# Kernel optimization log

Hardware: AMD Instinct MI355X
Metric: run time of the kernel (lower is better)

The kernel has to match this reference:

```python
import jax, jax.numpy as jnp
import numpy as np

DEPTH = 4
SCALE = 1.0


def _exp_levels(v, depth):
    # Tensor-algebra exponential of a linear segment with increment v: level k = v^{(x)k} / k!
    # v: (B, C); returns tuple of (B, C^k) for k=1..depth
    B = v.shape[0]
    levels = [v]
    for k in range(2, depth + 1):
        levels.append((levels[-1][:, :, None] * v[:, None, :]).reshape(B, -1) / k)
    return tuple(levels)


def _chen_step(levels, v, depth):
    # Chen's identity: S_new = S (x) exp(v), flattened per level.
    e = _exp_levels(v, depth)
    B = v.shape[0]
    new = []
    for k in range(1, depth + 1):
        acc = levels[k - 1] + e[k - 1]
        for i in range(1, k):
            acc = acc + (levels[i - 1][:, :, None] * e[k - i - 1][:, None, :]).reshape(B, -1)
        new.append(acc)
    return tuple(new)


def signature(path, depth):
    # path: (B, T, C) -> concatenated signature levels (B, C + C^2 + ... + C^depth)
    dx = path[:, 1:] - path[:, :-1]          # (B, T-1, C)
    init = _exp_levels(dx[:, 0], depth)      # signature of first segment
    rest = jnp.moveaxis(dx[:, 1:], 0, 1)     # (T-2, B, C)

    def step(lv, v):
        return _chen_step(lv, v, depth), None

    final, _ = jax.lax.scan(step, init, rest)
    return jnp.concatenate(final, axis=-1)


def setup_inputs() -> dict:
    key = jax.random.key(0)
    k1, k2, k3 = jax.random.split(key, 3)
    N, B, T, C = 4096, 1024, 256, 10
    original = jax.random.normal(k1, (N, T, C), dtype=jnp.float32) * 0.1
    generated = jax.random.normal(k2, (B, T, C), dtype=jnp.float32) * 0.1
    sample_idx = jax.random.permutation(k3, N)[:B].astype(jnp.int64)  # sample without replacement
    return {"original": original, "generated": generated, "sample_idx": sample_idx}


def reference(original, generated, sample_idx):
    sig_orig = signature(original, DEPTH)                  # (N, D)
    selected = sig_orig[sample_idx]                        # (B, D)
    sig_gen = signature(generated, DEPTH)                  # (B, D)
    diff = jnp.mean(selected, axis=0) - jnp.mean(sig_gen, axis=0)
    return jnp.linalg.norm(diff) * SCALE
```

## Files before the change

kernel.cpp:

```cpp
#include <hip/hip_runtime.h>

#define T_LEN 256
#define C_DIM 10
#define NSTEP 255
#define BSZ   1024
#define NPAIR 1024
#define D1 10
#define D2 100
#define D3 1000
#define DTOT 11110
#define PATH_ELEMS (T_LEN * C_DIM)
#define DX_ELEMS (NSTEP * C_DIM)
#define DXROW 12

typedef float f32x2 __attribute__((ext_vector_type(2)));
typedef float f32x4 __attribute__((ext_vector_type(4)));

#define PK_FMA(d, a, b) \
    asm("v_pk_fma_f32 %0, %1, %2, %0" : "+v"(d) : "v"(a), "v"(b))
#define PK_FMA_B0(d, a, b) \
    asm("v_pk_fma_f32 %0, %1, %2, %0 op_sel:[0,0,0] op_sel_hi:[0,1,1]" \
        : "+v"(d) : "v"(a), "v"(b))
#define PK_FMA_B1(d, a, b) \
    asm("v_pk_fma_f32 %0, %1, %2, %0 op_sel:[1,0,0] op_sel_hi:[1,1,1]" \
        : "+v"(d) : "v"(a), "v"(b))
#define PK_FMA_B0N(d, a, b, c) \
    asm("v_pk_fma_f32 %0, %1, %2, %3 op_sel:[0,0,0] op_sel_hi:[0,1,1]" \
        : "=v"(d) : "v"(a), "v"(b), "v"(c))
#define PK_FMA_B1N(d, a, b, c) \
    asm("v_pk_fma_f32 %0, %1, %2, %3 op_sel:[1,0,0] op_sel_hi:[1,1,1]" \
        : "=v"(d) : "v"(a), "v"(b), "v"(c))
#define PK_FMA_S1B0N(d, a, b, c) \
    asm("v_pk_fma_f32 %0, %1, %2, %3 op_sel:[0,0,0] op_sel_hi:[1,0,1]" \
        : "=v"(d) : "v"(a), "v"(b), "v"(c))
#define PK_FMA_S1B1N(d, a, b, c) \
    asm("v_pk_fma_f32 %0, %1, %2, %3 op_sel:[0,1,0] op_sel_hi:[1,1,1]" \
        : "=v"(d) : "v"(a), "v"(b), "v"(c))
#define PK_FMA_S1B0(d, a, b) \
    asm("v_pk_fma_f32 %0, %1, %2, %0 op_sel:[0,0,0] op_sel_hi:[1,0,1]" \
        : "+v"(d) : "v"(a), "v"(b))
#define PK_FMA_S1B1(d, a, b) \
    asm("v_pk_fma_f32 %0, %1, %2, %0 op_sel:[0,1,0] op_sel_hi:[1,1,1]" \
        : "+v"(d) : "v"(a), "v"(b))
#define PK_MUL_HALF(d, a) \
    asm("v_pk_mul_f32 %0, %1, 0.5 op_sel:[0,0] op_sel_hi:[1,0]" \
        : "=v"(d) : "v"(a))

__global__ __launch_bounds__(256)
void sig_accum_kernel(
    const float* __restrict__ original,
    const float* __restrict__ generated,
    const int* __restrict__ sample_idx,
    float* __restrict__ ws, int nrep, int store_mode)
{
    const int tid  = threadIdx.x;
    const int bp   = blockIdx.x;
    const int b    = bp >> 1;
    const int pass = bp & 1;
    const float sgn = pass ? 1.0f : -1.0f;

    __shared__ float s_dx[NSTEP * DXROW];

    const float* path = pass
        ? original + (size_t)sample_idx[b] * PATH_ELEMS
        : generated + (size_t)b * PATH_ELEMS;

    for (int idx = tid; idx < DX_ELEMS; idx += 256) {
        int t = idx / C_DIM, c = idx - t * C_DIM;
        s_dx[t * DXROW + c] = path[idx + C_DIM] - path[idx];
    }
    __syncthreads();

    const int mbase = 2 * tid;
    const int k0  = mbase / 100;
    const int ij0 = mbase - k0 * 100;
    const int ia  = ij0 / 10;
    const int j0  = ij0 - ia * 10;

    float s1a = 0.0f;
    f32x2 s2p = {0.0f, 0.0f};
    f32x2 s3p[2] = {{0.0f, 0.0f}, {0.0f, 0.0f}};
    f32x2 acc2[4][5];
    #pragma unroll
    for (int r = 0; r < 4; ++r)
        #pragma unroll
        for (int i = 0; i < 5; ++i) acc2[r][i] = (f32x2){0.0f, 0.0f};

    if (tid < 250) {
        const float* vrow = s_dx;
        #pragma unroll 2
        for (int t = 0; t < NSTEP; ++t, vrow += DXROW) {
            const f32x4 va = *(const f32x4*)(vrow);
            const f32x4 vb = *(const f32x4*)(vrow + 4);
            const f32x2 vc = *(const f32x2*)(vrow + 8);
            const f32x2 vjp = *(const f32x2*)(vrow + j0);
            const float via = vrow[ia];
            f32x2 vkp;
            vkp.x = vrow[k0];
            vkp.y = vrow[k0 + 5];

            const f32x2 vv2[5] = {va.xy, va.zw, vb.xy, vb.zw, vc};

            const float t3  = fmaf(via, 0.5f, s1a);
            const float t1b = fmaf(via, 0.25f, s1a) * (1.0f / 3.0f);
            const float t2b = fmaf(via, (1.0f / 3.0f), s1a) * 0.5f;
            f32x2 pA; pA.x = t1b; pA.y = t2b;
            f32x2 pT; pT.x = t3;  pT.y = t3;

            f32x2 vkhp;
            PK_MUL_HALF(vkhp, vkp);

            f32x2 a2p, b2p;
            PK_FMA_B0N(a2p, pA, vjp, s2p);
            PK_FMA_B1N(b2p, pA, vjp, s2p);
            PK_FMA_B0(s2p, pT, vjp);

            f32x2 a3xp, a3yp;
            PK_FMA_S1B0N(a3xp, a2p, vkhp, s3p[0]);
            PK_FMA_S1B1N(a3yp, a2p, vkhp, s3p[1]);
            PK_FMA_S1B0(s3p[0], b2p, vkp);
            PK_FMA_S1B1(s3p[1], b2p, vkp);

            #pragma unroll
            for (int i = 0; i < 5; ++i) {
                PK_FMA_B0(acc2[0][i], a3xp, vv2[i]);
                PK_FMA_B1(acc2[1][i], a3xp, vv2[i]);
                PK_FMA_B0(acc2[2][i], a3yp, vv2[i]);
                PK_FMA_B1(acc2[3][i], a3yp, vv2[i]);
            }
            s1a += via;
        }
    }

    if (store_mode) {
        float* row = ws + (size_t)bp * DTOT;
        if (tid < D1)
            row[tid] = sgn * (path[(T_LEN - 1) * C_DIM + tid] - path[tid]);
        if (tid < 50) {
            row[D1 + ij0]     = sgn * s2p[0];
            row[D1 + ij0 + 1] = sgn * s2p[1];
        }
        if (tid < 250) {
            #pragma unroll
            for (int ch = 0; ch < 2; ++ch) {
                const int kk = k0 + 5 * ch;
                #pragma unroll
                for (int q = 0; q < 2; ++q) {
                    const int idx3 = (ij0 + q) * 10 + kk;
                    row[D1 + D2 + idx3] = sgn * s3p[ch][q];
                    float* p4 = row + D1 + D2 + D3 + (size_t)idx3 * 10;
                    #pragma unroll
                    for (int i = 0; i < 5; ++i)
                        *(f32x2*)&p4[2 * i] = sgn * acc2[ch * 2 + q][i];
                }
            }
        }
    } else {
        float* base = ws + (size_t)(b % nrep) * DTOT;
        if (tid < D1)
            atomicAdd(&base[tid],
                      sgn * (path[(T_LEN - 1) * C_DIM + tid] - path[tid]));
        if (tid < 50) {
            atomicAdd(&base[D1 + ij0],     sgn * s2p[0]);
            atomicAdd(&base[D1 + ij0 + 1], sgn * s2p[1]);
        }
        if (tid < 250) {
            #pragma unroll
            for (int ch = 0; ch < 2; ++ch) {
                const int kk = k0 + 5 * ch;
                #pragma unroll
                for (int q = 0; q < 2; ++q) {
                    const int idx3 = (ij0 + q) * 10 + kk;
                    atomicAdd(&base[D1 + D2 + idx3], sgn * s3p[ch][q]);
                    #pragma unroll
                    for (int l = 0; l < 10; ++l)
                        atomicAdd(&base[D1 + D2 + D3 + idx3 * 10 + l],
                                  sgn * acc2[ch * 2 + q][l >> 1][l & 1]);
                }
            }
        }
    }
}

__global__ __launch_bounds__(256) void sig_sum_kernel(
    const float* __restrict__ ws, float* __restrict__ accvec)
{
    const int d2 = blockIdx.x * 256 + threadIdx.x;
    if (d2 >= DTOT / 2) return;
    const float* p = ws + (size_t)(blockIdx.y * 32) * DTOT + 2 * d2;
    float sx = 0.0f, sy = 0.0f;
    #pragma unroll
    for (int r = 0; r < 32; ++r) {
        const float2 v = *(const float2*)(p + (size_t)r * DTOT);
        sx += v.x; sy += v.y;
    }
    atomicAdd(&accvec[2 * d2], sx);
    atomicAdd(&accvec[2 * d2 + 1], sy);
}

__global__ __launch_bounds__(256) void sig_sumsq_kernel(
    const float* __restrict__ accvec, float* __restrict__ sumsq,
    unsigned int* __restrict__ counter, float* __restrict__ out, int nblocks)
{
    const int d = blockIdx.x * 256 + threadIdx.x;
    float s = 0.0f;
    if (d < DTOT) { float v = accvec[d]; s = v * v; }
    for (int off = 32; off > 0; off >>= 1) s += __shfl_down(s, off, 64);
    __shared__ float red[4];
    __shared__ unsigned int lastflag;
    if ((threadIdx.x & 63) == 0) red[threadIdx.x >> 6] = s;
    __syncthreads();
    if (threadIdx.x == 0) {
        atomicAdd(sumsq, red[0] + red[1] + red[2] + red[3]);
        __threadfence();
        lastflag = (atomicAdd(counter, 1u) == (unsigned int)(nblocks - 1));
    }
    __syncthreads();
    if (threadIdx.x == 0 && lastflag) {
        __threadfence();
        out[0] = sqrtf(*(volatile float*)sumsq) * (1.0f / (float)BSZ);
    }
}

__global__ __launch_bounds__(256) void sig_reduce_kernel(
    const float* __restrict__ ws, int nrows, float* __restrict__ sumsq,
    unsigned int* __restrict__ counter, float* __restrict__ out, int nblocks)
{
    const int d = blockIdx.x * 256 + threadIdx.x;
    float s = 0.0f;
    if (d < DTOT) {
        for (int r = 0; r < nrows; ++r) s += ws[(size_t)r * DTOT + d];
        s = s * s;
    }
    for (int off = 32; off > 0; off >>= 1) s += __shfl_down(s, off, 64);
    __shared__ float red[4];
    __shared__ unsigned int lastflag;
    if ((threadIdx.x & 63) == 0) red[threadIdx.x >> 6] = s;
    __syncthreads();
    if (threadIdx.x == 0) {
        atomicAdd(sumsq, red[0] + red[1] + red[2] + red[3]);
        __threadfence();
        lastflag = (atomicAdd(counter, 1u) == (unsigned int)(nblocks - 1));
    }
    __syncthreads();
    if (threadIdx.x == 0 && lastflag) {
        __threadfence();
        out[0] = sqrtf(*(volatile float*)sumsq) * (1.0f / (float)BSZ);
    }
}

extern "C" void kernel_launch(void* const* d_in, const int* in_sizes, int n_in,
                              void* d_out, int out_size, void* d_ws, size_t ws_size,
                              hipStream_t stream) {
    const float* original   = (const float*)d_in[0];
    const float* generated  = (const float*)d_in[1];
    const int*   sample_idx = (const int*)d_in[2];
    float* out = (float*)d_out;
    float* ws  = (float*)d_ws;

    const size_t need_split = ((size_t)(2 * NPAIR + 1) * DTOT + 2) * sizeof(float);
    const size_t need_store = ((size_t)(NPAIR + 1) * DTOT + 2) * sizeof(float);

    if (ws_size >= need_split) {
        float* accvec = ws + (size_t)2 * NPAIR * DTOT;
        float* sumsq  = accvec + DTOT;
        unsigned int* counter = (unsigned int*)(sumsq + 1);
        hipMemsetAsync(accvec, 0, (DTOT + 2) * sizeof(float), stream);
        sig_accum_kernel<<<2 * NPAIR, 256, 0, stream>>>(original, generated,
                                                        sample_idx, ws, 1, 1);
        dim3 g1((DTOT / 2 + 255) / 256, 2 * NPAIR / 32);
        sig_sum_kernel<<<g1, 256, 0, stream>>>(ws, accvec);
        const int nb2 = (DTOT + 255) / 256;
        sig_sumsq_kernel<<<nb2, 256, 0, stream>>>(accvec, sumsq, counter, out, nb2);
    } else if (ws_size >= need_store) {
        float* accvec = ws + (size_t)NPAIR * DTOT;
        float* sumsq  = accvec + DTOT;
        unsigned int* counter = (unsigned int*)(sumsq + 1);
        hipMemsetAsync(ws, 0, need_store, stream);
        sig_accum_kernel<<<2 * NPAIR, 256, 0, stream>>>(original, generated,
                                                        sample_idx, ws, NPAIR, 0);
        dim3 g1((DTOT / 2 + 255) / 256, NPAIR / 32);
        sig_sum_kernel<<<g1, 256, 0, stream>>>(ws, accvec);
        const int nb2 = (DTOT + 255) / 256;
        sig_sumsq_kernel<<<nb2, 256, 0, stream>>>(accvec, sumsq, counter, out, nb2);
    } else {
        int nrep = 1;
        if (ws_size >= ((size_t)64 * DTOT + 2) * sizeof(float)) nrep = 64;
        else if (ws_size >= ((size_t)8 * DTOT + 2) * sizeof(float)) nrep = 8;
        float* sumsq = ws + (size_t)nrep * DTOT;
        unsigned int* counter = (unsigned int*)(sumsq + 1);
        hipMemsetAsync(ws, 0, ((size_t)nrep * DTOT + 2) * sizeof(float), stream);
        sig_accum_kernel<<<2 * NPAIR, 256, 0, stream>>>(original, generated,
                                                        sample_idx, ws, nrep, 0);
        const int nb2 = (DTOT + 255) / 256;
        sig_reduce_kernel<<<nb2, 256, 0, stream>>>(ws, nrep, sumsq, counter, out, nb2);
    }
}
```

Before: 282.9 us.

## Precompute path increments in a separate kernel and read uniform rows from global

Adds a pre-pass kernel that writes padded path increments (12 floats per step) to workspace. The accumulation kernel then fills shared memory with float4 copies and reads the wave-uniform full increment row straight from global memory, likely turning those loads into cached scalar or broadcast loads instead of LDS reads. This is meant to cut LDS traffic in the hot loop. The cost is an extra kernel launch and an extra round trip of the increment data through global memory, and the path only runs when the workspace is large enough.

```diff
diff --git a/kernel.cpp b/kernel.cpp
--- a/kernel.cpp
+++ b/kernel.cpp
@@ -12,12 +12,11 @@
 #define PATH_ELEMS (T_LEN * C_DIM)
 #define DX_ELEMS (NSTEP * C_DIM)
 #define DXROW 12
+#define DXBLK (NSTEP * DXROW)
 
 typedef float f32x2 __attribute__((ext_vector_type(2)));
 typedef float f32x4 __attribute__((ext_vector_type(4)));
 
-#define PK_FMA(d, a, b) \
-    asm("v_pk_fma_f32 %0, %1, %2, %0" : "+v"(d) : "v"(a), "v"(b))
 #define PK_FMA_B0(d, a, b) \
     asm("v_pk_fma_f32 %0, %1, %2, %0 op_sel:[0,0,0] op_sel_hi:[0,1,1]" \
         : "+v"(d) : "v"(a), "v"(b))
@@ -47,10 +46,34 @@
         : "=v"(d) : "v"(a))
 
 __global__ __launch_bounds__(256)
+void sig_dx_kernel(const float* __restrict__ original,
+                   const float* __restrict__ generated,
+                   const int* __restrict__ sample_idx,
+                   float* __restrict__ gdx)
+{
+    const int tid = threadIdx.x;
+    const int bp  = blockIdx.x;
+    const int b   = bp >> 1;
+    const int pass = bp & 1;
+    const float* path = pass
+        ? original + (size_t)sample_idx[b] * PATH_ELEMS
+        : generated + (size_t)b * PATH_ELEMS;
+    float* outp = gdx + (size_t)bp * DXBLK;
+    for (int idx = tid; idx < DXBLK; idx += 256) {
+        const int t = idx / DXROW, c = idx - t * DXROW;
+        float v = 0.0f;
+        if (c < C_DIM) v = path[t * C_DIM + c + C_DIM] - path[t * C_DIM + c];
+        outp[idx] = v;
+    }
+}
+
+template<int USE_GDX>
+__global__ __launch_bounds__(256)
 void sig_accum_kernel(
     const float* __restrict__ original,
     const float* __restrict__ generated,
     const int* __restrict__ sample_idx,
+    const float* __restrict__ gdx,
     float* __restrict__ ws, int nrep, int store_mode)
 {
     const int tid  = threadIdx.x;
@@ -59,15 +82,21 @@
     const int pass = bp & 1;
     const float sgn = pass ? 1.0f : -1.0f;
 
-    __shared__ float s_dx[NSTEP * DXROW];
+    __shared__ __align__(16) float s_dx[DXBLK];
 
     const float* path = pass
         ? original + (size_t)sample_idx[b] * PATH_ELEMS
         : generated + (size_t)b * PATH_ELEMS;
 
-    for (int idx = tid; idx < DX_ELEMS; idx += 256) {
-        int t = idx / C_DIM, c = idx - t * C_DIM;
-        s_dx[t * DXROW + c] = path[idx + C_DIM] - path[idx];
+    if (USE_GDX) {
+        const float4* src = (const float4*)(gdx + (size_t)bp * DXBLK);
+        float4* dst = (float4*)s_dx;
+        for (int i = tid; i < DXBLK / 4; i += 256) dst[i] = src[i];
+    } else {
+        for (int idx = tid; idx < DX_ELEMS; idx += 256) {
+            int t = idx / C_DIM, c = idx - t * C_DIM;
+            s_dx[t * DXROW + c] = path[idx + C_DIM] - path[idx];
+        }
     }
     __syncthreads();
 
@@ -88,11 +117,12 @@
 
     if (tid < 250) {
         const float* vrow = s_dx;
+        const float* gu = USE_GDX ? (gdx + (size_t)bp * DXBLK) : s_dx;
         #pragma unroll 2
-        for (int t = 0; t < NSTEP; ++t, vrow += DXROW) {
-            const f32x4 va = *(const f32x4*)(vrow);
-            const f32x4 vb = *(const f32x4*)(vrow + 4);
-            const f32x2 vc = *(const f32x2*)(vrow + 8);
+        for (int t = 0; t < NSTEP; ++t, vrow += DXROW, gu += DXROW) {
+            const f32x4 va = *(const f32x4*)(gu);
+            const f32x4 vb = *(const f32x4*)(gu + 4);
+            const f32x2 vc = *(const f32x2*)(gu + 8);
             const f32x2 vjp = *(const f32x2*)(vrow + j0);
             const float via = vrow[ia];
             f32x2 vkp;
@@ -258,16 +288,33 @@
     float* out = (float*)d_out;
     float* ws  = (float*)d_ws;
 
+    const size_t need_gdx   = ((size_t)2 * NPAIR * (DTOT + DXBLK) + DTOT + 2) * sizeof(float);
     const size_t need_split = ((size_t)(2 * NPAIR + 1) * DTOT + 2) * sizeof(float);
     const size_t need_store = ((size_t)(NPAIR + 1) * DTOT + 2) * sizeof(float);
 
-    if (ws_size >= need_split) {
+    if (ws_size >= need_gdx) {
+        float* gdx    = ws + (size_t)2 * NPAIR * DTOT;
+        float* accvec = gdx + (size_t)2 * NPAIR * DXBLK;
+        float* sumsq  = accvec + DTOT;
+        unsigned int* counter = (unsigned int*)(sumsq + 1);
+        hipMemsetAsync(accvec, 0, (DTOT + 2) * sizeof(float), stream);
+        sig_dx_kernel<<<2 * NPAIR, 256, 0, stream>>>(original, generated,
+                                                     sample_idx, gdx);
+        sig_accum_kernel<1><<<2 * NPAIR, 256, 0, stream>>>(original, generated,
+                                                           sample_idx, gdx,
+                                                           ws, 1, 1);
+        dim3 g1((DTOT / 2 + 255) / 256, 2 * NPAIR / 32);
+        sig_sum_kernel<<<g1, 256, 0, stream>>>(ws, accvec);
+        const int nb2 = (DTOT + 255) / 256;
+        sig_sumsq_kernel<<<nb2, 256, 0, stream>>>(accvec, sumsq, counter, out, nb2);
+    } else if (ws_size >= need_split) {
         float* accvec = ws + (size_t)2 * NPAIR * DTOT;
         float* sumsq  = accvec + DTOT;
         unsigned int* counter = (unsigned int*)(sumsq + 1);
         hipMemsetAsync(accvec, 0, (DTOT + 2) * sizeof(float), stream);
-        sig_accum_kernel<<<2 * NPAIR, 256, 0, stream>>>(original, generated,
-                                                        sample_idx, ws, 1, 1);
+        sig_accum_kernel<0><<<2 * NPAIR, 256, 0, stream>>>(original, generated,
+                                                           sample_idx, nullptr,
+                                                           ws, 1, 1);
         dim3 g1((DTOT / 2 + 255) / 256, 2 * NPAIR / 32);
         sig_sum_kernel<<<g1, 256, 0, stream>>>(ws, accvec);
         const int nb2 = (DTOT + 255) / 256;
@@ -277,8 +324,9 @@
         float* sumsq  = accvec + DTOT;
         unsigned int* counter = (unsigned int*)(sumsq + 1);
         hipMemsetAsync(ws, 0, need_store, stream);
-        sig_accum_kernel<<<2 * NPAIR, 256, 0, stream>>>(original, generated,
-                                                        sample_idx, ws, NPAIR, 0);
+        sig_accum_kernel<0><<<2 * NPAIR, 256, 0, stream>>>(original, generated,
+                                                           sample_idx, nullptr,
+                                                           ws, NPAIR, 0);
         dim3 g1((DTOT / 2 + 255) / 256, NPAIR / 32);
         sig_sum_kernel<<<g1, 256, 0, stream>>>(ws, accvec);
         const int nb2 = (DTOT + 255) / 256;
@@ -290,8 +338,9 @@
         float* sumsq = ws + (size_t)nrep * DTOT;
         unsigned int* counter = (unsigned int*)(sumsq + 1);
         hipMemsetAsync(ws, 0, ((size_t)nrep * DTOT + 2) * sizeof(float), stream);
-        sig_accum_kernel<<<2 * NPAIR, 256, 0, stream>>>(original, generated,
-                                                        sample_idx, ws, nrep, 0);
+        sig_accum_kernel<0><<<2 * NPAIR, 256, 0, stream>>>(original, generated,
+                                                           sample_idx, nullptr,
+                                                           ws, nrep, 0);
         const int nb2 = (DTOT + 255) / 256;
         sig_reduce_kernel<<<nb2, 256, 0, stream>>>(ws, nrep, sumsq, counter, out, nb2);
     }
```

After: 309.5 us. 9.4% more time.

## Process two output slices per thread with 128-thread blocks; fold memset into kernel

Applied to the files above, without the earlier changes.

Each thread now computes two independent level-3/4 slices (A and B) while sharing the per-step shared-memory loads of the increment row, and blocks shrink from 256 to 128 threads. This halves the redundant LDS traffic per FMA and gives each thread more independent work to hide latency. The separate hipMemsetAsync of the accumulator is replaced by block 0 zeroing it inside the accum kernel, removing one launch. Register pressure roughly doubles, which may lower occupancy.

```diff
diff --git a/kernel.cpp b/kernel.cpp
--- a/kernel.cpp
+++ b/kernel.cpp
@@ -16,8 +16,6 @@
 typedef float f32x2 __attribute__((ext_vector_type(2)));
 typedef float f32x4 __attribute__((ext_vector_type(4)));
 
-#define PK_FMA(d, a, b) \
-    asm("v_pk_fma_f32 %0, %1, %2, %0" : "+v"(d) : "v"(a), "v"(b))
 #define PK_FMA_B0(d, a, b) \
     asm("v_pk_fma_f32 %0, %1, %2, %0 op_sel:[0,0,0] op_sel_hi:[0,1,1]" \
         : "+v"(d) : "v"(a), "v"(b))
@@ -46,12 +44,14 @@
     asm("v_pk_mul_f32 %0, %1, 0.5 op_sel:[0,0] op_sel_hi:[1,0]" \
         : "=v"(d) : "v"(a))
 
-__global__ __launch_bounds__(256)
+__global__ __launch_bounds__(128)
 void sig_accum_kernel(
     const float* __restrict__ original,
     const float* __restrict__ generated,
     const int* __restrict__ sample_idx,
-    float* __restrict__ ws, int nrep, int store_mode)
+    float* __restrict__ ws,
+    float* __restrict__ accinit,
+    int nrep, int store_mode)
 {
     const int tid  = threadIdx.x;
     const int bp   = blockIdx.x;
@@ -59,76 +59,119 @@
     const int pass = bp & 1;
     const float sgn = pass ? 1.0f : -1.0f;
 
-    __shared__ float s_dx[NSTEP * DXROW];
+    __shared__ __align__(16) float s_dx[NSTEP * DXROW];
+
+    if (accinit != nullptr && bp == 0) {
+        for (int i = tid; i < DTOT + 2; i += 128) accinit[i] = 0.0f;
+    }
 
     const float* path = pass
         ? original + (size_t)sample_idx[b] * PATH_ELEMS
         : generated + (size_t)b * PATH_ELEMS;
 
-    for (int idx = tid; idx < DX_ELEMS; idx += 256) {
+    for (int idx = tid; idx < DX_ELEMS; idx += 128) {
         int t = idx / C_DIM, c = idx - t * C_DIM;
         s_dx[t * DXROW + c] = path[idx + C_DIM] - path[idx];
     }
     __syncthreads();
 
-    const int mbase = 2 * tid;
-    const int k0  = mbase / 100;
-    const int ij0 = mbase - k0 * 100;
-    const int ia  = ij0 / 10;
-    const int j0  = ij0 - ia * 10;
-
-    float s1a = 0.0f;
-    f32x2 s2p = {0.0f, 0.0f};
-    f32x2 s3p[2] = {{0.0f, 0.0f}, {0.0f, 0.0f}};
-    f32x2 acc2[4][5];
+    const int mA  = 2 * tid;
+    const int mB  = 2 * tid + 250;
+    const int k0A = mA / 100, ijA = mA - 100 * k0A;
+    const int iaA = ijA / 10, j0A = ijA - 10 * iaA;
+    const int k0B = mB / 100, ijB = mB - 100 * k0B;
+    const int iaB = ijB / 10, j0B = ijB - 10 * iaB;
+
+    float s1A = 0.0f, s1B = 0.0f;
+    f32x2 s2A = {0.0f, 0.0f}, s2B = {0.0f, 0.0f};
+    f32x2 s3A[2] = {{0.0f, 0.0f}, {0.0f, 0.0f}};
+    f32x2 s3B[2] = {{0.0f, 0.0f}, {0.0f, 0.0f}};
+    f32x2 accA[4][5], accB[4][5];
     #pragma unroll
     for (int r = 0; r < 4; ++r)
         #pragma unroll
-        for (int i = 0; i < 5; ++i) acc2[r][i] = (f32x2){0.0f, 0.0f};
-
-    if (tid < 250) {
+        for (int i = 0; i < 5; ++i) {
+            accA[r][i] = (f32x2){0.0f, 0.0f};
+            accB[r][i] = (f32x2){0.0f, 0.0f};
+        }
+
+    if (tid < 125) {
         const float* vrow = s_dx;
         #pragma unroll 2
         for (int t = 0; t < NSTEP; ++t, vrow += DXROW) {
             const f32x4 va = *(const f32x4*)(vrow);
             const f32x4 vb = *(const f32x4*)(vrow + 4);
             const f32x2 vc = *(const f32x2*)(vrow + 8);
-            const f32x2 vjp = *(const f32x2*)(vrow + j0);
-            const float via = vrow[ia];
-            f32x2 vkp;
-            vkp.x = vrow[k0];
-            vkp.y = vrow[k0 + 5];
-
             const f32x2 vv2[5] = {va.xy, va.zw, vb.xy, vb.zw, vc};
 
-            const float t3  = fmaf(via, 0.5f, s1a);
-            const float t1b = fmaf(via, 0.25f, s1a) * (1.0f / 3.0f);
-            const float t2b = fmaf(via, (1.0f / 3.0f), s1a) * 0.5f;
-            f32x2 pA; pA.x = t1b; pA.y = t2b;
-            f32x2 pT; pT.x = t3;  pT.y = t3;
-
-            f32x2 vkhp;
-            PK_MUL_HALF(vkhp, vkp);
-
-            f32x2 a2p, b2p;
-            PK_FMA_B0N(a2p, pA, vjp, s2p);
-            PK_FMA_B1N(b2p, pA, vjp, s2p);
-            PK_FMA_B0(s2p, pT, vjp);
-
-            f32x2 a3xp, a3yp;
-            PK_FMA_S1B0N(a3xp, a2p, vkhp, s3p[0]);
-            PK_FMA_S1B1N(a3yp, a2p, vkhp, s3p[1]);
-            PK_FMA_S1B0(s3p[0], b2p, vkp);
-            PK_FMA_S1B1(s3p[1], b2p, vkp);
-
-            #pragma unroll
-            for (int i = 0; i < 5; ++i) {
-                PK_FMA_B0(acc2[0][i], a3xp, vv2[i]);
-                PK_FMA_B1(acc2[1][i], a3xp, vv2[i]);
-                PK_FMA_B0(acc2[2][i], a3yp, vv2[i]);
-                PK_FMA_B1(acc2[3][i], a3yp, vv2[i]);
-            }
-            s1a += via;
+            {
+                const f32x2 vj = *(const f32x2*)(vrow + j0A);
+                const float via = vrow[iaA];
+                f32x2 vk; vk.x = vrow[k0A]; vk.y = vrow[k0A + 5];
+
+                const float t3  = fmaf(via, 0.5f, s1A);
+                const float t1b = fmaf(via, 0.25f, s1A) * (1.0f / 3.0f);
+                const float t2b = fmaf(via, (1.0f / 3.0f), s1A) * 0.5f;
+                f32x2 pA_; pA_.x = t1b; pA_.y = t2b;
+                f32x2 pT;  pT.x = t3;   pT.y = t3;
+
+                f32x2 vkh;
+                PK_MUL_HALF(vkh, vk);
+
+                f32x2 a2, b2;
+                PK_FMA_B0N(a2, pA_, vj, s2A);
+                PK_FMA_B1N(b2, pA_, vj, s2A);
+                PK_FMA_B0(s2A, pT, vj);
+
+                f32x2 a3x, a3y;
+                PK_FMA_S1B0N(a3x, a2, vkh, s3A[0]);
+                PK_FMA_S1B1N(a3y, a2, vkh, s3A[1]);
+                PK_FMA_S1B0(s3A[0], b2, vk);
+                PK_FMA_S1B1(s3A[1], b2, vk);
+
+                #pragma unroll
+                for (int i = 0; i < 5; ++i) {
+                    PK_FMA_B0(accA[0][i], a3x, vv2[i]);
+                    PK_FMA_B1(accA[1][i], a3x, vv2[i]);
+                    PK_FMA_B0(accA[2][i], a3y, vv2[i]);
+                    PK_FMA_B1(accA[3][i], a3y, vv2[i]);
+                }
+                s1A += via;
+            }
+            {
+                const f32x2 vj = *(const f32x2*)(vrow + j0B);
+                const float via = vrow[iaB];
+                f32x2 vk; vk.x = vrow[k0B]; vk.y = vrow[k0B + 5];
+
+                const float t3  = fmaf(via, 0.5f, s1B);
+                const float t1b = fmaf(via, 0.25f, s1B) * (1.0f / 3.0f);
+                const float t2b = fmaf(via, (1.0f / 3.0f), s1B) * 0.5f;
+                f32x2 pA_; pA_.x = t1b; pA_.y = t2b;
+                f32x2 pT;  pT.x = t3;   pT.y = t3;
+
+                f32x2 vkh;
+                PK_MUL_HALF(vkh, vk);
+
+                f32x2 a2, b2;
+                PK_FMA_B0N(a2, pA_, vj, s2B);
+                PK_FMA_B1N(b2, pA_, vj, s2B);
+                PK_FMA_B0(s2B, pT, vj);
+
+                f32x2 a3x, a3y;
+                PK_FMA_S1B0N(a3x, a2, vkh, s3B[0]);
+                PK_FMA_S1B1N(a3y, a2, vkh, s3B[1]);
+                PK_FMA_S1B0(s3B[0], b2, vk);
+                PK_FMA_S1B1(s3B[1], b2, vk);
+
+                #pragma unroll
+                for (int i = 0; i < 5; ++i) {
+                    PK_FMA_B0(accB[0][i], a3x, vv2[i]);
+                    PK_FMA_B1(accB[1][i], a3x, vv2[i]);
+                    PK_FMA_B0(accB[2][i], a3y, vv2[i]);
+                    PK_FMA_B1(accB[3][i], a3y, vv2[i]);
+                }
+                s1B += via;
+            }
         }
     }
 
@@ -137,21 +180,34 @@
         if (tid < D1)
             row[tid] = sgn * (path[(T_LEN - 1) * C_DIM + tid] - path[tid]);
         if (tid < 50) {
-            row[D1 + ij0]     = sgn * s2p[0];
-            row[D1 + ij0 + 1] = sgn * s2p[1];
-        }
-        if (tid < 250) {
+            row[D1 + ijA]     = sgn * s2A[0];
+            row[D1 + ijA + 1] = sgn * s2A[1];
+        }
+        if (tid < 125) {
             #pragma unroll
             for (int ch = 0; ch < 2; ++ch) {
-                const int kk = k0 + 5 * ch;
+                const int kkA = k0A + 5 * ch;
                 #pragma unroll
                 for (int q = 0; q < 2; ++q) {
-                    const int idx3 = (ij0 + q) * 10 + kk;
-                    row[D1 + D2 + idx3] = sgn * s3p[ch][q];
+                    const int idx3 = (ijA + q) * 10 + kkA;
+                    row[D1 + D2 + idx3] = sgn * s3A[ch][q];
                     float* p4 = row + D1 + D2 + D3 + (size_t)idx3 * 10;
                     #pragma unroll
                     for (int i = 0; i < 5; ++i)
-                        *(f32x2*)&p4[2 * i] = sgn * acc2[ch * 2 + q][i];
+                        *(f32x2*)&p4[2 * i] = sgn * accA[ch * 2 + q][i];
+                }
+            }
+            #pragma unroll
+            for (int ch = 0; ch < 2; ++ch) {
+                const int kkB = k0B + 5 * ch;
+                #pragma unroll
+                for (int q = 0; q < 2; ++q) {
+                    const int idx3 = (ijB + q) * 10 + kkB;
+                    row[D1 + D2 + idx3] = sgn * s3B[ch][q];
+                    float* p4 = row + D1 + D2 + D3 + (size_t)idx3 * 10;
+                    #pragma unroll
+                    for (int i = 0; i < 5; ++i)
+                        *(f32x2*)&p4[2 * i] = sgn * accB[ch * 2 + q][i];
                 }
             }
         }
@@ -161,21 +217,34 @@
             atomicAdd(&base[tid],
                       sgn * (path[(T_LEN - 1) * C_DIM + tid] - path[tid]));
         if (tid < 50) {
-            atomicAdd(&base[D1 + ij0],     sgn * s2p[0]);
-            atomicAdd(&base[D1 + ij0 + 1], sgn * s2p[1]);
-        }
-        if (tid < 250) {
+            atomicAdd(&base[D1 + ijA],     sgn * s2A[0]);
+            atomicAdd(&base[D1 + ijA + 1], sgn * s2A[1]);
+        }
+        if (tid < 125) {
             #pragma unroll
             for (int ch = 0; ch < 2; ++ch) {
-                const int kk = k0 + 5 * ch;
+                const int kkA = k0A + 5 * ch;
                 #pragma unroll
                 for (int q = 0; q < 2; ++q) {
-                    const int idx3 = (ij0 + q) * 10 + kk;
-                    atomicAdd(&base[D1 + D2 + idx3], sgn * s3p[ch][q]);
+                    const int idx3 = (ijA + q) * 10 + kkA;
+                    atomicAdd(&base[D1 + D2 + idx3], sgn * s3A[ch][q]);
                     #pragma unroll
                     for (int l = 0; l < 10; ++l)
                         atomicAdd(&base[D1 + D2 + D3 + idx3 * 10 + l],
-                                  sgn * acc2[ch * 2 + q][l >> 1][l & 1]);
+                                  sgn * accA[ch * 2 + q][l >> 1][l & 1]);
+                }
+            }
+            #pragma unroll
+            for (int ch = 0; ch < 2; ++ch) {
+                const int kkB = k0B + 5 * ch;
+                #pragma unroll
+                for (int q = 0; q < 2; ++q) {
+                    const int idx3 = (ijB + q) * 10 + kkB;
+                    atomicAdd(&base[D1 + D2 + idx3], sgn * s3B[ch][q]);
+                    #pragma unroll
+                    for (int l = 0; l < 10; ++l)
+                        atomicAdd(&base[D1 + D2 + D3 + idx3 * 10 + l],
+                                  sgn * accB[ch * 2 + q][l >> 1][l & 1]);
                 }
             }
         }
@@ -265,9 +334,9 @@
         float* accvec = ws + (size_t)2 * NPAIR * DTOT;
         float* sumsq  = accvec + DTOT;
         unsigned int* counter = (unsigned int*)(sumsq + 1);
-        hipMemsetAsync(accvec, 0, (DTOT + 2) * sizeof(float), stream);
-        sig_accum_kernel<<<2 * NPAIR, 256, 0, stream>>>(original, generated,
-                                                        sample_idx, ws, 1, 1);
+        sig_accum_kernel<<<2 * NPAIR, 128, 0, stream>>>(original, generated,
+                                                        sample_idx, ws, accvec,
+                                                        1, 1);
         dim3 g1((DTOT / 2 + 255) / 256, 2 * NPAIR / 32);
         sig_sum_kernel<<<g1, 256, 0, stream>>>(ws, accvec);
         const int nb2 = (DTOT + 255) / 256;
@@ -277,8 +346,9 @@
         float* sumsq  = accvec + DTOT;
         unsigned int* counter = (unsigned int*)(sumsq + 1);
         hipMemsetAsync(ws, 0, need_store, stream);
-        sig_accum_kernel<<<2 * NPAIR, 256, 0, stream>>>(original, generated,
-                                                        sample_idx, ws, NPAIR, 0);
+        sig_accum_kernel<<<2 * NPAIR, 128, 0, stream>>>(original, generated,
+                                                        sample_idx, ws, nullptr,
+                                                        NPAIR, 0);
         dim3 g1((DTOT / 2 + 255) / 256, NPAIR / 32);
         sig_sum_kernel<<<g1, 256, 0, stream>>>(ws, accvec);
         const int nb2 = (DTOT + 255) / 256;
@@ -290,8 +360,9 @@
         float* sumsq = ws + (size_t)nrep * DTOT;
         unsigned int* counter = (unsigned int*)(sumsq + 1);
         hipMemsetAsync(ws, 0, ((size_t)nrep * DTOT + 2) * sizeof(float), stream);
-        sig_accum_kernel<<<2 * NPAIR, 256, 0, stream>>>(original, generated,
-                                                        sample_idx, ws, nrep, 0);
+        sig_accum_kernel<<<2 * NPAIR, 128, 0, stream>>>(original, generated,
+                                                        sample_idx, ws, nullptr,
+                                                        nrep, 0);
         const int nb2 = (DTOT + 255) / 256;
         sig_reduce_kernel<<<nb2, 256, 0, stream>>>(ws, nrep, sumsq, counter, out, nb2);
     }
```

New measurement: 279.2 us. No clear change (-1.3%).
